# Optimization experiments

Measured on AMD Instinct MI355X. Metric: run time of the kernel, lower is better.

Reference implementation:

```python
import jax, jax.numpy as jnp
import numpy as np

NUM_ITER = 3
EPS = 1e-7


def squash(t, axis=-1):
    sq = jnp.sum(t * t, axis=axis, keepdims=True)
    safe_norm = jnp.sqrt(sq + EPS)
    return (sq / (1.0 + sq)) * (t / safe_norm)


def setup_inputs() -> dict:
    key = jax.random.key(0)
    k1, k2 = jax.random.split(key)
    B, D, P, O, I = 256, 10, 1152, 16, 8
    x = jax.random.normal(k1, (B, P, I), dtype=jnp.float32)
    W = 0.01 * jax.random.normal(k2, (1, D, P, O, I), dtype=jnp.float32)
    return {"x": x, "W": W}


def reference(x, W):
    B = x.shape[0]
    D, P = W.shape[1], W.shape[2]
    # u_hat: [B, D, P, O]  (W @ u with u = x[:,None,:, :,None])
    u_hat = jnp.einsum("zdpoi,bpi->bdpo", W, x)
    temp_u_hat = jax.lax.stop_gradient(u_hat)
    b = jnp.zeros((B, D, P, 1), dtype=u_hat.dtype)
    for _ in range(NUM_ITER - 1):
        c = jax.nn.softmax(b, axis=1)          # [B, D, P, 1]
        s = jnp.sum(c * temp_u_hat, axis=2)    # [B, D, O]
        v = squash(s)                          # [B, D, O]
        uv = jnp.einsum("bdpo,bdo->bdp", temp_u_hat, v)[..., None]
        b = b + uv
    c = jax.nn.softmax(b, axis=1)
    s = jnp.sum(c * u_hat, axis=2)
    return squash(s)  # [B, D, O]
```

## Files before the change

kernel.cpp:

```cpp
#include <hip/hip_runtime.h>

namespace {

constexpr int BATCH = 256;
constexpr int DCAPS = 10;
constexpr int PCAPS = 1152;
constexpr int ODIM  = 16;
constexpr int IDIM  = 8;
constexpr float EPS_ = 1e-7f;

constexpr int NPBLK = 128;
constexpr int PPB   = PCAPS / NPBLK;
constexpr int BPG   = 2;
constexpr int GPB   = 16;
constexpr int BT    = GPB * BPG;
constexpr int NBB   = BATCH / BT;
constexpr int SDO   = BATCH * DCAPS * ODIM;
constexpr float LOG2E = 1.44269504088896f;

__device__ __forceinline__ float rsum16(float v)
{
    v += __int_as_float(__builtin_amdgcn_update_dpp(
        0, __float_as_int(v), 0x121, 0xF, 0xF, true));
    v += __int_as_float(__builtin_amdgcn_update_dpp(
        0, __float_as_int(v), 0x122, 0xF, 0xF, true));
    v += __int_as_float(__builtin_amdgcn_update_dpp(
        0, __float_as_int(v), 0x124, 0xF, 0xF, true));
    v += __int_as_float(__builtin_amdgcn_update_dpp(
        0, __float_as_int(v), 0x128, 0xF, 0xF, true));
    return v;
}

__device__ __forceinline__ float dot8(const float4& wa, const float4& wb,
                                      const float4& xa, const float4& xb)
{
    float acc = wa.x * xa.x;
    acc = fmaf(wa.y, xa.y, acc);
    acc = fmaf(wa.z, xa.z, acc);
    acc = fmaf(wa.w, xa.w, acc);
    acc = fmaf(wb.x, xb.x, acc);
    acc = fmaf(wb.y, xb.y, acc);
    acc = fmaf(wb.z, xb.z, acc);
    acc = fmaf(wb.w, xb.w, acc);
    return acc;
}

template <int NV>
__global__ __launch_bounds__(256, 4)
void route_kernel(const float* __restrict__ x, const float* __restrict__ W,
                  const float* __restrict__ v0, const float* __restrict__ v1,
                  float* __restrict__ part)
{
    const int tid  = threadIdx.x;
    const int g    = tid >> 4;
    const int o    = tid & 15;
    const int pBlk = blockIdx.x % NPBLK;
    const int bBlk = blockIdx.x / NPBLK;
    const int b0   = bBlk * BT + g * BPG;
    const int p0   = pBlk * PPB;

    float vr[BPG][DCAPS];
    if constexpr (NV >= 1) {
#pragma unroll
        for (int bb = 0; bb < BPG; ++bb)
#pragma unroll
            for (int d = 0; d < DCAPS; ++d) {
                float t = v0[((size_t)(b0 + bb) * DCAPS + d) * ODIM + o];
                if constexpr (NV == 2)
                    t += v1[((size_t)(b0 + bb) * DCAPS + d) * ODIM + o];
                vr[bb][d] = t * LOG2E;
            }
    }

    float s_acc[BPG][DCAPS];
#pragma unroll
    for (int bb = 0; bb < BPG; ++bb)
#pragma unroll
        for (int d = 0; d < DCAPS; ++d) s_acc[bb][d] = 0.f;

    for (int pp = 0; pp < PPB; ++pp) {
        const int p = p0 + pp;

        float4 xa[BPG], xb[BPG];
#pragma unroll
        for (int bb = 0; bb < BPG; ++bb) {
            const float4* xp = reinterpret_cast<const float4*>(
                x + ((size_t)(b0 + bb) * PCAPS + p) * IDIM);
            xa[bb] = xp[0];
            xb[bb] = xp[1];
        }

        float uh[BPG][DCAPS];
#pragma unroll
        for (int d = 0; d < DCAPS; ++d) {
            const float4* wp = reinterpret_cast<const float4*>(
                W + (((size_t)d * PCAPS + p) * ODIM + o) * IDIM);
            const float4 wa = wp[0];
            const float4 wb = wp[1];
#pragma unroll
            for (int bb = 0; bb < BPG; ++bb)
                uh[bb][d] = dot8(wa, wb, xa[bb], xb[bb]);
        }

        if constexpr (NV == 0) {
#pragma unroll
            for (int bb = 0; bb < BPG; ++bb)
#pragma unroll
                for (int d = 0; d < DCAPS; ++d)
                    s_acc[bb][d] = fmaf(0.1f, uh[bb][d], s_acc[bb][d]);
        } else {
            float e[BPG][DCAPS];
            float den[BPG];
#pragma unroll
            for (int bb = 0; bb < BPG; ++bb) den[bb] = 0.f;
#pragma unroll
            for (int bb = 0; bb < BPG; ++bb)
#pragma unroll
                for (int d = 0; d < DCAPS; ++d) {
                    const float l = rsum16(uh[bb][d] * vr[bb][d]);
                    const float t = exp2f(l);
                    e[bb][d] = t;
                    den[bb] += t;
                }
#pragma unroll
            for (int bb = 0; bb < BPG; ++bb) {
                const float inv = 1.0f / den[bb];
#pragma unroll
                for (int d = 0; d < DCAPS; ++d)
                    s_acc[bb][d] = fmaf(e[bb][d] * inv, uh[bb][d], s_acc[bb][d]);
            }
        }
    }

#pragma unroll
    for (int bb = 0; bb < BPG; ++bb)
#pragma unroll
        for (int d = 0; d < DCAPS; ++d)
            part[((size_t)pBlk * BATCH + (b0 + bb)) * (DCAPS * ODIM)
                 + d * ODIM + o] = s_acc[bb][d];
}

template <int NP>
__global__ __launch_bounds__(256)
void squash_kernel(const float* __restrict__ part, float* __restrict__ out)
{
    constexpr int CPC = NP / 8;
    const int tid = threadIdx.x;
    const int u   = tid >> 5;
    const int l   = tid & 31;
    const int cg  = l >> 2;
    const int q   = l & 3;
    const int gu  = blockIdx.x * 8 + u;

    float4 acc = make_float4(0, 0, 0, 0);
    for (int k = 0; k < CPC; ++k) {
        const int c = cg * CPC + k;
        const float4 p4 = reinterpret_cast<const float4*>(
            part + (size_t)c * SDO + (size_t)gu * ODIM)[q];
        acc.x += p4.x; acc.y += p4.y; acc.z += p4.z; acc.w += p4.w;
    }

    __shared__ float4 sred[8][8][4];
    __shared__ float4 sfin[8][4];
    __shared__ float  nrm[8][4];
    __shared__ float  sscale[8];
    sred[u][cg][q] = acc;
    __syncthreads();

    if (cg == 0) {
        float4 s = sred[u][0][q];
#pragma unroll
        for (int c2 = 1; c2 < 8; ++c2) {
            const float4 t = sred[u][c2][q];
            s.x += t.x; s.y += t.y; s.z += t.z; s.w += t.w;
        }
        sfin[u][q] = s;
        nrm[u][q]  = s.x * s.x + s.y * s.y + s.z * s.z + s.w * s.w;
    }
    __syncthreads();
    if (l == 0) {
        const float sq = nrm[u][0] + nrm[u][1] + nrm[u][2] + nrm[u][3];
        sscale[u] = (sq / (1.0f + sq)) / sqrtf(sq + EPS_);
    }
    __syncthreads();
    if (cg == 0) {
        float4 s = sfin[u][q];
        const float sc = sscale[u];
        s.x *= sc; s.y *= sc; s.z *= sc; s.w *= sc;
        reinterpret_cast<float4*>(out)[(size_t)gu * 4 + q] = s;
    }
}

}

extern "C" void kernel_launch(void* const* d_in, const int* in_sizes, int n_in,
                              void* d_out, int out_size, void* d_ws, size_t ws_size,
                              hipStream_t stream)
{
    const float* x = (const float*)d_in[0];
    const float* W = (const float*)d_in[1];
    float* out = (float*)d_out;

    float* v0   = (float*)d_ws;
    float* v1   = v0 + SDO;
    float* part = v1 + SDO;

    const dim3 rblk(256);
    const dim3 rgrid(NPBLK * NBB);
    const dim3 sblk(256);
    const dim3 sgrid(BATCH * DCAPS / 8);

    route_kernel<0><<<rgrid, rblk, 0, stream>>>(x, W, nullptr, nullptr, part);
    squash_kernel<NPBLK><<<sgrid, sblk, 0, stream>>>(part, v0);

    route_kernel<1><<<rgrid, rblk, 0, stream>>>(x, W, v0, nullptr, part);
    squash_kernel<NPBLK><<<sgrid, sblk, 0, stream>>>(part, v1);

    route_kernel<2><<<rgrid, rblk, 0, stream>>>(x, W, v0, v1, part);
    squash_kernel<NPBLK><<<sgrid, sblk, 0, stream>>>(part, out);
}
```

Measured before the change: 202.7 us.

## Repack W into p-major layout and raise p-block count when workspace allows

Adds a repack kernel that rewrites W from [D,P,O,I] into [P,D,O,I] order, so each p step of the routing kernel reads one contiguous region. When workspace is large enough it also splits P into 192 blocks instead of 128, giving more blocks for parallelism at the cost of a larger partial-sum buffer. The repack adds an extra launch and a full read and write of W on every call, and the squash kernel must reduce more partials.

```diff
diff --git a/kernel.cpp b/kernel.cpp
--- a/kernel.cpp
+++ b/kernel.cpp
@@ -9,13 +9,12 @@
 constexpr int IDIM  = 8;
 constexpr float EPS_ = 1e-7f;
 
-constexpr int NPBLK = 128;
-constexpr int PPB   = PCAPS / NPBLK;
-constexpr int BPG   = 2;
-constexpr int GPB   = 16;
-constexpr int BT    = GPB * BPG;
-constexpr int NBB   = BATCH / BT;
-constexpr int SDO   = BATCH * DCAPS * ODIM;
+constexpr int BPG = 2;
+constexpr int GPB = 16;
+constexpr int BT  = GPB * BPG;
+constexpr int NBB = BATCH / BT;
+constexpr int SDO = BATCH * DCAPS * ODIM;
+constexpr int WSZ = DCAPS * PCAPS * ODIM * IDIM;
 constexpr float LOG2E = 1.44269504088896f;
 
 __device__ __forceinline__ float rsum16(float v)
@@ -45,12 +44,27 @@
     return acc;
 }
 
-template <int NV>
+__global__ __launch_bounds__(256)
+void repack_kernel(const float* __restrict__ W, float* __restrict__ Wp)
+{
+    const int k  = blockIdx.x * 256 + threadIdx.x;
+    const int i4 = k & 1;
+    const int o  = (k >> 1) & 15;
+    const int pd = k >> 5;
+    const int d  = pd % DCAPS;
+    const int p  = pd / DCAPS;
+    reinterpret_cast<float4*>(Wp)[k] =
+        reinterpret_cast<const float4*>(W)[
+            ((((size_t)d * PCAPS + p) * ODIM + o) << 1) + i4];
+}
+
+template <int NV, int NPBLK, bool PACKED>
 __global__ __launch_bounds__(256, 4)
-void route_kernel(const float* __restrict__ x, const float* __restrict__ W,
+void route_kernel(const float* __restrict__ x, const float* __restrict__ Wp,
                   const float* __restrict__ v0, const float* __restrict__ v1,
                   float* __restrict__ part)
 {
+    constexpr int PPB = PCAPS / NPBLK;
     const int tid  = threadIdx.x;
     const int g    = tid >> 4;
     const int o    = tid & 15;
@@ -91,15 +105,30 @@
         }
 
         float uh[BPG][DCAPS];
-#pragma unroll
-        for (int d = 0; d < DCAPS; ++d) {
-            const float4* wp = reinterpret_cast<const float4*>(
-                W + (((size_t)d * PCAPS + p) * ODIM + o) * IDIM);
-            const float4 wa = wp[0];
-            const float4 wb = wp[1];
-#pragma unroll
-            for (int bb = 0; bb < BPG; ++bb)
-                uh[bb][d] = dot8(wa, wb, xa[bb], xb[bb]);
+        if constexpr (PACKED) {
+            const float* wbase = Wp + (size_t)p * (DCAPS * ODIM * IDIM)
+                                    + o * IDIM;
+#pragma unroll
+            for (int d = 0; d < DCAPS; ++d) {
+                const float4* wv = reinterpret_cast<const float4*>(
+                    wbase + d * (ODIM * IDIM));
+                const float4 wa = wv[0];
+                const float4 wb = wv[1];
+#pragma unroll
+                for (int bb = 0; bb < BPG; ++bb)
+                    uh[bb][d] = dot8(wa, wb, xa[bb], xb[bb]);
+            }
+        } else {
+#pragma unroll
+            for (int d = 0; d < DCAPS; ++d) {
+                const float4* wv = reinterpret_cast<const float4*>(
+                    Wp + (((size_t)d * PCAPS + p) * ODIM + o) * IDIM);
+                const float4 wa = wv[0];
+                const float4 wb = wv[1];
+#pragma unroll
+                for (int bb = 0; bb < BPG; ++bb)
+                    uh[bb][d] = dot8(wa, wb, xa[bb], xb[bb]);
+            }
         }
 
         if constexpr (NV == 0) {
@@ -191,6 +220,25 @@
     }
 }
 
+template <int NPBLK, bool PACKED>
+void run_all(const float* x, const float* W, const float* Wp,
+             float* v0, float* v1, float* part, float* out, hipStream_t stream)
+{
+    const dim3 blk(256);
+    const dim3 rgrid(NPBLK * NBB);
+    const dim3 sgrid(BATCH * DCAPS / 8);
+    const float* Wk = PACKED ? Wp : W;
+
+    route_kernel<0, NPBLK, PACKED><<<rgrid, blk, 0, stream>>>(x, Wk, nullptr, nullptr, part);
+    squash_kernel<NPBLK><<<sgrid, blk, 0, stream>>>(part, v0);
+
+    route_kernel<1, NPBLK, PACKED><<<rgrid, blk, 0, stream>>>(x, Wk, v0, nullptr, part);
+    squash_kernel<NPBLK><<<sgrid, blk, 0, stream>>>(part, v1);
+
+    route_kernel<2, NPBLK, PACKED><<<rgrid, blk, 0, stream>>>(x, Wk, v0, v1, part);
+    squash_kernel<NPBLK><<<sgrid, blk, 0, stream>>>(part, out);
+}
+
 }
 
 extern "C" void kernel_launch(void* const* d_in, const int* in_sizes, int n_in,
@@ -203,19 +251,19 @@
 
     float* v0   = (float*)d_ws;
     float* v1   = v0 + SDO;
-    float* part = v1 + SDO;
-
-    const dim3 rblk(256);
-    const dim3 rgrid(NPBLK * NBB);
-    const dim3 sblk(256);
-    const dim3 sgrid(BATCH * DCAPS / 8);
-
-    route_kernel<0><<<rgrid, rblk, 0, stream>>>(x, W, nullptr, nullptr, part);
-    squash_kernel<NPBLK><<<sgrid, sblk, 0, stream>>>(part, v0);
-
-    route_kernel<1><<<rgrid, rblk, 0, stream>>>(x, W, v0, nullptr, part);
-    squash_kernel<NPBLK><<<sgrid, sblk, 0, stream>>>(part, v1);
-
-    route_kernel<2><<<rgrid, rblk, 0, stream>>>(x, W, v0, v1, part);
-    squash_kernel<NPBLK><<<sgrid, sblk, 0, stream>>>(part, out);
-}
+    float* Wp   = v1 + SDO;
+    float* part = Wp + WSZ;
+
+    const size_t needA = ((size_t)2 * SDO + WSZ + (size_t)192 * SDO) * sizeof(float);
+    const size_t needB = ((size_t)2 * SDO + WSZ + (size_t)128 * SDO) * sizeof(float);
+
+    if (ws_size >= needA) {
+        repack_kernel<<<dim3(WSZ / 4 / 256), dim3(256), 0, stream>>>(W, Wp);
+        run_all<192, true>(x, W, Wp, v0, v1, part, out, stream);
+    } else if (ws_size >= needB) {
+        repack_kernel<<<dim3(WSZ / 4 / 256), dim3(256), 0, stream>>>(W, Wp);
+        run_all<128, true>(x, W, Wp, v0, v1, part, out, stream);
+    } else {
+        run_all<128, false>(x, W, W, v0, v1, Wp, out, stream);
+    }
+}
```

Result: slower. 210.8 us (+4.0%).

## Compute u_hat with split-bf16 MFMA and keep an fp32 fallback path

Applied to the files above, without the earlier changes.

Each call first splits W and x into bf16 hi/lo pairs. The routing kernels then compute u_hat with 16x16x32 bf16 MFMA, using three products (hh, lh, hl) to approximate fp32 accuracy. The p-capsule split changes to 96 blocks, and a lane-shuffle reduction replaces the DPP reduction. The aim is to move the dot-product work onto the matrix cores, at the cost of two extra split kernels, more workspace, wasted MFMA lanes (the x operand is zero outside the diagonal k-group), and bf16-split precision error. If the workspace is too small, it falls back to an fp32 kernel that now handles 4 batches per group.

```diff
diff --git a/kernel.cpp b/kernel.cpp
--- a/kernel.cpp
+++ b/kernel.cpp
@@ -1,4 +1,5 @@
 #include <hip/hip_runtime.h>
+#include <hip/hip_bf16.h>
 
 namespace {
 
@@ -8,15 +9,144 @@
 constexpr int ODIM  = 16;
 constexpr int IDIM  = 8;
 constexpr float EPS_ = 1e-7f;
-
-constexpr int NPBLK = 128;
-constexpr int PPB   = PCAPS / NPBLK;
-constexpr int BPG   = 2;
-constexpr int GPB   = 16;
-constexpr int BT    = GPB * BPG;
-constexpr int NBB   = BATCH / BT;
-constexpr int SDO   = BATCH * DCAPS * ODIM;
+constexpr int SDO = BATCH * DCAPS * ODIM;
 constexpr float LOG2E = 1.44269504088896f;
+
+typedef __attribute__((ext_vector_type(8))) short short8_t;
+typedef __attribute__((ext_vector_type(4))) float f32x4;
+
+__device__ __forceinline__ ushort f2bf_bits(float f)
+{
+    __hip_bfloat16 h = __float2bfloat16(f);
+    return *reinterpret_cast<ushort*>(&h);
+}
+__device__ __forceinline__ float bfbits2f(ushort u)
+{
+    __hip_bfloat16 h = *reinterpret_cast<__hip_bfloat16*>(&u);
+    return __bfloat162float(h);
+}
+
+__global__ __launch_bounds__(256)
+void split_kernel(const float* __restrict__ src, ushort* __restrict__ hi,
+                  ushort* __restrict__ lo, int n4)
+{
+    const int i = blockIdx.x * 256 + threadIdx.x;
+    if (i >= n4) return;
+    const float4 w = reinterpret_cast<const float4*>(src)[i];
+    ushort4 h, l;
+    h.x = f2bf_bits(w.x); l.x = f2bf_bits(w.x - bfbits2f(h.x));
+    h.y = f2bf_bits(w.y); l.y = f2bf_bits(w.y - bfbits2f(h.y));
+    h.z = f2bf_bits(w.z); l.z = f2bf_bits(w.z - bfbits2f(h.z));
+    h.w = f2bf_bits(w.w); l.w = f2bf_bits(w.w - bfbits2f(h.w));
+    reinterpret_cast<ushort4*>(hi)[i] = h;
+    reinterpret_cast<ushort4*>(lo)[i] = l;
+}
+
+template <int NV, int NPBLK>
+__global__ __launch_bounds__(256, 2)
+void route_mfma(const ushort* __restrict__ xh, const ushort* __restrict__ xl,
+                const ushort* __restrict__ wh, const ushort* __restrict__ wl,
+                const float* __restrict__ v0, const float* __restrict__ v1,
+                float* __restrict__ part)
+{
+    constexpr int PPB = PCAPS / NPBLK;
+    constexpr int TPW = PPB / 4;
+    const int tid  = threadIdx.x;
+    const int l    = tid & 63;
+    const int w    = tid >> 6;
+    const int pBlk = blockIdx.x % NPBLK;
+    const int bBlk = blockIdx.x / NPBLK;
+    const int kgrp = l >> 4;
+    const int n    = l & 15;
+    const int bsub = n >> 2;
+    const int psub = n & 3;
+    const int b    = bBlk * 16 + w * 4 + bsub;
+    const int o0   = kgrp * 4;
+
+    f32x4 vr[DCAPS];
+    if constexpr (NV >= 1) {
+#pragma unroll
+        for (int d = 0; d < DCAPS; ++d) {
+            const float4 t = *reinterpret_cast<const float4*>(
+                v0 + ((size_t)b * DCAPS + d) * ODIM + o0);
+            f32x4 v = {t.x, t.y, t.z, t.w};
+            if constexpr (NV == 2) {
+                const float4 u = *reinterpret_cast<const float4*>(
+                    v1 + ((size_t)b * DCAPS + d) * ODIM + o0);
+                v.x += u.x; v.y += u.y; v.z += u.z; v.w += u.w;
+            }
+            vr[d] = v * LOG2E;
+        }
+    }
+
+    const f32x4 zero4 = {0.f, 0.f, 0.f, 0.f};
+    f32x4 s_acc[DCAPS];
+#pragma unroll
+    for (int d = 0; d < DCAPS; ++d) s_acc[d] = zero4;
+
+    const bool xact = (kgrp == psub);
+
+    for (int t = 0; t < TPW; ++t) {
+        const int p0 = pBlk * PPB + t * 4;
+
+        short8_t bxh = {0,0,0,0,0,0,0,0};
+        short8_t bxl = {0,0,0,0,0,0,0,0};
+        if (xact) {
+            const size_t xo = ((size_t)b * PCAPS + p0 + psub) * IDIM;
+            bxh = *reinterpret_cast<const short8_t*>(xh + xo);
+            bxl = *reinterpret_cast<const short8_t*>(xl + xo);
+        }
+
+        f32x4 acc[DCAPS];
+#pragma unroll
+        for (int d = 0; d < DCAPS; ++d) {
+            const size_t wo = (((size_t)d * PCAPS + p0 + kgrp) * ODIM + n) * IDIM;
+            const short8_t awh = *reinterpret_cast<const short8_t*>(wh + wo);
+            const short8_t awl = *reinterpret_cast<const short8_t*>(wl + wo);
+            f32x4 a = zero4;
+            a = __builtin_amdgcn_mfma_f32_16x16x32_bf16(awh, bxh, a, 0, 0, 0);
+            a = __builtin_amdgcn_mfma_f32_16x16x32_bf16(awl, bxh, a, 0, 0, 0);
+            a = __builtin_amdgcn_mfma_f32_16x16x32_bf16(awh, bxl, a, 0, 0, 0);
+            acc[d] = a;
+        }
+
+        if constexpr (NV == 0) {
+#pragma unroll
+            for (int d = 0; d < DCAPS; ++d) s_acc[d] += 0.1f * acc[d];
+        } else {
+            float e[DCAPS];
+            float den = 0.f;
+#pragma unroll
+            for (int d = 0; d < DCAPS; ++d) {
+                const f32x4 pr = acc[d] * vr[d];
+                float t2 = pr.x + pr.y + pr.z + pr.w;
+                t2 += __shfl_xor(t2, 16);
+                t2 += __shfl_xor(t2, 32);
+                const float ex = exp2f(t2);
+                e[d] = ex;
+                den += ex;
+            }
+            const float inv = 1.0f / den;
+#pragma unroll
+            for (int d = 0; d < DCAPS; ++d)
+                s_acc[d] += (e[d] * inv) * acc[d];
+        }
+    }
+
+#pragma unroll
+    for (int d = 0; d < DCAPS; ++d) {
+        f32x4 s = s_acc[d];
+        s.x += __shfl_xor(s.x, 1); s.x += __shfl_xor(s.x, 2);
+        s.y += __shfl_xor(s.y, 1); s.y += __shfl_xor(s.y, 2);
+        s.z += __shfl_xor(s.z, 1); s.z += __shfl_xor(s.z, 2);
+        s.w += __shfl_xor(s.w, 1); s.w += __shfl_xor(s.w, 2);
+        if (psub == 0) {
+            float4 st; st.x = s.x; st.y = s.y; st.z = s.z; st.w = s.w;
+            *reinterpret_cast<float4*>(
+                part + (((size_t)pBlk * BATCH + b) * DCAPS + d) * ODIM + o0) = st;
+        }
+    }
+}
 
 __device__ __forceinline__ float rsum16(float v)
 {
@@ -46,11 +176,12 @@
 }
 
 template <int NV>
-__global__ __launch_bounds__(256, 4)
-void route_kernel(const float* __restrict__ x, const float* __restrict__ W,
-                  const float* __restrict__ v0, const float* __restrict__ v1,
-                  float* __restrict__ part)
-{
+__global__ __launch_bounds__(256, 2)
+void route_fp32(const float* __restrict__ x, const float* __restrict__ W,
+                const float* __restrict__ v0, const float* __restrict__ v1,
+                float* __restrict__ part)
+{
+    constexpr int NPBLK = 128, PPB = 9, BPG = 4, BT = 64;
     const int tid  = threadIdx.x;
     const int g    = tid >> 4;
     const int o    = tid & 15;
@@ -71,7 +202,6 @@
                 vr[bb][d] = t * LOG2E;
             }
     }
-
     float s_acc[BPG][DCAPS];
 #pragma unroll
     for (int bb = 0; bb < BPG; ++bb)
@@ -80,28 +210,24 @@
 
     for (int pp = 0; pp < PPB; ++pp) {
         const int p = p0 + pp;
-
         float4 xa[BPG], xb[BPG];
 #pragma unroll
         for (int bb = 0; bb < BPG; ++bb) {
             const float4* xp = reinterpret_cast<const float4*>(
                 x + ((size_t)(b0 + bb) * PCAPS + p) * IDIM);
-            xa[bb] = xp[0];
-            xb[bb] = xp[1];
-        }
-
+            xa[bb] = xp[0]; xb[bb] = xp[1];
+        }
         float uh[BPG][DCAPS];
 #pragma unroll
         for (int d = 0; d < DCAPS; ++d) {
-            const float4* wp = reinterpret_cast<const float4*>(
+            const float4* wv = reinterpret_cast<const float4*>(
                 W + (((size_t)d * PCAPS + p) * ODIM + o) * IDIM);
-            const float4 wa = wp[0];
-            const float4 wb = wp[1];
+            const float4 wa = wv[0];
+            const float4 wb = wv[1];
 #pragma unroll
             for (int bb = 0; bb < BPG; ++bb)
                 uh[bb][d] = dot8(wa, wb, xa[bb], xb[bb]);
         }
-
         if constexpr (NV == 0) {
 #pragma unroll
             for (int bb = 0; bb < BPG; ++bb)
@@ -117,10 +243,9 @@
             for (int bb = 0; bb < BPG; ++bb)
 #pragma unroll
                 for (int d = 0; d < DCAPS; ++d) {
-                    const float l = rsum16(uh[bb][d] * vr[bb][d]);
-                    const float t = exp2f(l);
-                    e[bb][d] = t;
-                    den[bb] += t;
+                    const float lg = rsum16(uh[bb][d] * vr[bb][d]);
+                    const float t = exp2f(lg);
+                    e[bb][d] = t; den[bb] += t;
                 }
 #pragma unroll
             for (int bb = 0; bb < BPG; ++bb) {
@@ -131,7 +256,6 @@
             }
         }
     }
-
 #pragma unroll
     for (int bb = 0; bb < BPG; ++bb)
 #pragma unroll
@@ -159,14 +283,12 @@
             part + (size_t)c * SDO + (size_t)gu * ODIM)[q];
         acc.x += p4.x; acc.y += p4.y; acc.z += p4.z; acc.w += p4.w;
     }
-
     __shared__ float4 sred[8][8][4];
     __shared__ float4 sfin[8][4];
     __shared__ float  nrm[8][4];
     __shared__ float  sscale[8];
     sred[u][cg][q] = acc;
     __syncthreads();
-
     if (cg == 0) {
         float4 s = sred[u][0][q];
 #pragma unroll
@@ -201,21 +323,45 @@
     const float* W = (const float*)d_in[1];
     float* out = (float*)d_out;
 
-    float* v0   = (float*)d_ws;
-    float* v1   = v0 + SDO;
-    float* part = v1 + SDO;
-
-    const dim3 rblk(256);
-    const dim3 rgrid(NPBLK * NBB);
-    const dim3 sblk(256);
+    constexpr int NPB  = 96;
+    constexpr int WELT = DCAPS * PCAPS * ODIM * IDIM;
+    constexpr int XELT = BATCH * PCAPS * IDIM;
+
+    float* v0 = (float*)d_ws;
+    float* v1 = v0 + SDO;
+    ushort* wh = (ushort*)(v1 + SDO);
+    ushort* wl = wh + WELT;
+    ushort* xh = wl + WELT;
+    ushort* xl = xh + XELT;
+    float* partM = (float*)(xl + XELT);
+
+    const size_t needM = ((size_t)2 * SDO + WELT + XELT
+                          + (size_t)NPB * SDO) * sizeof(float);
+
+    const dim3 blk(256);
     const dim3 sgrid(BATCH * DCAPS / 8);
 
-    route_kernel<0><<<rgrid, rblk, 0, stream>>>(x, W, nullptr, nullptr, part);
-    squash_kernel<NPBLK><<<sgrid, sblk, 0, stream>>>(part, v0);
-
-    route_kernel<1><<<rgrid, rblk, 0, stream>>>(x, W, v0, nullptr, part);
-    squash_kernel<NPBLK><<<sgrid, sblk, 0, stream>>>(part, v1);
-
-    route_kernel<2><<<rgrid, rblk, 0, stream>>>(x, W, v0, v1, part);
-    squash_kernel<NPBLK><<<sgrid, sblk, 0, stream>>>(part, out);
-}
+    if (ws_size >= needM) {
+        split_kernel<<<dim3((WELT / 4 + 255) / 256), blk, 0, stream>>>(W, wh, wl, WELT / 4);
+        split_kernel<<<dim3((XELT / 4 + 255) / 256), blk, 0, stream>>>(x, xh, xl, XELT / 4);
+
+        const dim3 rgrid(NPB * (BATCH / 16));
+        route_mfma<0, NPB><<<rgrid, blk, 0, stream>>>(xh, xl, wh, wl, nullptr, nullptr, partM);
+        squash_kernel<NPB><<<sgrid, blk, 0, stream>>>(partM, v0);
+
+        route_mfma<1, NPB><<<rgrid, blk, 0, stream>>>(xh, xl, wh, wl, v0, nullptr, partM);
+        squash_kernel<NPB><<<sgrid, blk, 0, stream>>>(partM, v1);
+
+        route_mfma<2, NPB><<<rgrid, blk, 0, stream>>>(xh, xl, wh, wl, v0, v1, partM);
+        squash_kernel<NPB><<<sgrid, blk, 0, stream>>>(partM, out);
+    } else {
+        float* partF = v1 + SDO;
+        const dim3 rgrid(128 * 4);
+        route_fp32<0><<<rgrid, blk, 0, stream>>>(x, W, nullptr, nullptr, partF);
+        squash_kernel<128><<<sgrid, blk, 0, stream>>>(partF, v0);
+        route_fp32<1><<<rgrid, blk, 0, stream>>>(x, W, v0, nullptr, partF);
+        squash_kernel<128><<<sgrid, blk, 0, stream>>>(partF, v1);
+        route_fp32<2><<<rgrid, blk, 0, stream>>>(x, W, v0, v1, partF);
+        squash_kernel<128><<<sgrid, blk, 0, stream>>>(partF, out);
+    }
+}
```

Measured after the change: 165.3 us. 1.23x faster.
